# Optimization experiments

Measured on AMD Instinct MI355X. Metric: run time of the kernel, lower is better.

Reference implementation:

```python
import jax, jax.numpy as jnp
import numpy as np

INF = 100000000.0
STRIDES = [8, 16, 32, 64, 128]
REGRESS_RANGES = [(-1.0, 64.0), (64.0, 128.0), (128.0, 256.0), (256.0, 512.0), (512.0, INF)]
IMG = 1024
RADIUS = 1.5
BACKGROUND = 80
NUM_GTS = 512


def setup_inputs() -> dict:
    key = jax.random.key(0)
    k1, k2, k3 = jax.random.split(key, 3)
    # valid gt boxes: centers in image, sizes 10..300, xyxy clipped to image
    cxcy = jax.random.uniform(k1, (NUM_GTS, 2), minval=0.0, maxval=float(IMG))
    wh = jax.random.uniform(k2, (NUM_GTS, 2), minval=10.0, maxval=300.0)
    x1y1 = jnp.clip(cxcy - wh / 2, 0.0, float(IMG))
    x2y2 = jnp.clip(cxcy + wh / 2, 0.0, float(IMG))
    gt_bboxes = jnp.concatenate([x1y1, x2y2], axis=-1)
    gt_labels = jax.random.randint(k3, (NUM_GTS,), 0, BACKGROUND)
    pts, rr, st = [], [], []
    for s, (lo, hi) in zip(STRIDES, REGRESS_RANGES):
        h = w = IMG // s
        y, x = np.meshgrid(np.arange(h), np.arange(w), indexing='ij')
        p = np.stack([x.reshape(-1) * s, y.reshape(-1) * s], axis=-1) + s // 2
        pts.append(p.astype(np.float32))
        rr.append(np.tile(np.array([lo, hi], np.float32), (h * w, 1)))
        st.append(np.full((h * w,), s * RADIUS, np.float32))
    points = jnp.asarray(np.concatenate(pts, 0))          # [N, 2]
    regress_ranges = jnp.asarray(np.concatenate(rr, 0))   # [N, 2]
    strides_pts = jnp.asarray(np.concatenate(st, 0))      # [N]
    return {"points": points, "regress_ranges": regress_ranges,
            "strides_pts": strides_pts, "gt_bboxes": gt_bboxes, "gt_labels": gt_labels}


def reference(points, regress_ranges, strides_pts, gt_bboxes, gt_labels):
    # FCOSTarget._get_target_single (center_sampling=True, no ignore boxes)
    N = points.shape[0]
    xs = points[:, 0:1]  # [N,1]
    ys = points[:, 1:2]
    areas = (gt_bboxes[:, 2] - gt_bboxes[:, 0]) * (gt_bboxes[:, 3] - gt_bboxes[:, 1])  # [G]
    # point-to-box distances, [N,G,4] = (left, top, right, bottom)
    l = xs - gt_bboxes[None, :, 0]
    t = ys - gt_bboxes[None, :, 1]
    r = gt_bboxes[None, :, 2] - xs
    b = gt_bboxes[None, :, 3] - ys
    bbox_targets = jnp.stack([l, t, r, b], axis=-1)  # [N,G,4]
    # center sampling: shrink gt box to stride*radius window around its center
    cx = (gt_bboxes[None, :, 0] + gt_bboxes[None, :, 2]) * 0.5  # [1,G]
    cy = (gt_bboxes[None, :, 1] + gt_bboxes[None, :, 3]) * 0.5
    rad = strides_pts[:, None]  # [N,1], already stride * radius
    x0 = jnp.maximum(cx - rad, gt_bboxes[None, :, 0])
    y0 = jnp.maximum(cy - rad, gt_bboxes[None, :, 1])
    x1 = jnp.minimum(cx + rad, gt_bboxes[None, :, 2])
    y1 = jnp.minimum(cy + rad, gt_bboxes[None, :, 3])
    center_bbox = jnp.stack([xs - x0, ys - y0, x1 - xs, y1 - ys], axis=-1)  # [N,G,4]
    inside_gt_bbox_mask = center_bbox.min(axis=-1) > 0  # [N,G]
    max_regress_distance = bbox_targets.max(axis=-1)  # [N,G]
    inside_regress_range = ((max_regress_distance >= regress_ranges[:, 0:1]) &
                            (max_regress_distance <= regress_ranges[:, 1:2]))
    # masked argmin over gt areas
    areas_masked = jnp.where(inside_gt_bbox_mask & inside_regress_range, areas[None, :], INF)
    min_area = areas_masked.min(axis=1)        # [N]
    min_area_inds = areas_masked.argmin(axis=1)  # [N]
    labels = jnp.where(min_area == INF, BACKGROUND, gt_labels[min_area_inds])
    bt = jnp.take_along_axis(bbox_targets, min_area_inds[:, None, None], axis=1)[:, 0, :]  # [N,4]
    label_weights = jnp.ones((N,), jnp.float32)
    return labels, bt, label_weights
```

## Files before the change

### kernel.cpp

```cpp
#include <hip/hip_runtime.h>

#define INF_AREA 100000000.0f
#define BACKGROUND_LBL 80
#define MAX_GTS 512
#define SPLIT 8

__global__ __launch_bounds__(256) void fcos_target_kernel(
    const float* __restrict__ points,
    const float* __restrict__ regress_ranges,
    const float* __restrict__ strides_pts,
    const float* __restrict__ gt_bboxes,
    const int*   __restrict__ gt_labels,
    float* __restrict__ out,
    int N, int M)
{
    __shared__ float4 sbox[MAX_GTS];
    __shared__ float4 saux[MAX_GTS];

    const float4* gtb4 = reinterpret_cast<const float4*>(gt_bboxes);
    for (int j = threadIdx.x; j < M; j += blockDim.x) {
        float4 b = gtb4[j];
        sbox[j] = b;
        float4 aux;
        aux.x = (b.z - b.x) * (b.w - b.y);
        aux.y = (b.x + b.z) * 0.5f;
        aux.z = (b.y + b.w) * 0.5f;
        aux.w = __int_as_float(gt_labels[j]);
        saux[j] = aux;
    }
    __syncthreads();

    int tid = blockIdx.x * blockDim.x + threadIdx.x;
    int i   = tid >> 3;
    int sub = tid & (SPLIT - 1);
    if (i >= N) return;

    float x   = points[i * 2 + 0];
    float y   = points[i * 2 + 1];
    float rr0 = regress_ranges[i * 2 + 0];
    float rr1 = regress_ranges[i * 2 + 1];
    float rad = strides_pts[i];

    float minA   = INF_AREA;
    int   minIdx = sub;

    for (int j = sub; j < M; j += SPLIT) {
        float4 bx = sbox[j];
        float4 ax = saux[j];
        float l = x - bx.x, t = y - bx.y, r = bx.z - x, b = bx.w - y;
        float mr = fmaxf(fmaxf(l, t), fmaxf(r, b));
        bool in_range = (mr >= rr0) && (mr <= rr1);
        float x0 = fmaxf(ax.y - rad, bx.x);
        float y0 = fmaxf(ax.z - rad, bx.y);
        float x1 = fminf(ax.y + rad, bx.z);
        float y1 = fminf(ax.z + rad, bx.w);
        float cmin = fminf(fminf(x - x0, y - y0), fminf(x1 - x, y1 - y));
        float a = (in_range && (cmin > 0.0f)) ? ax.x : INF_AREA;
        if (a < minA) { minA = a; minIdx = j; }
    }

    for (int off = 1; off < SPLIT; off <<= 1) {
        float oA = __shfl_xor(minA, off);
        int   oI = __shfl_xor(minIdx, off);
        if (oA < minA || (oA == minA && oI < minIdx)) { minA = oA; minIdx = oI; }
    }

    if (sub == 0) {
        float4 bb = sbox[minIdx];
        int lab = (minA == INF_AREA) ? BACKGROUND_LBL : __float_as_int(saux[minIdx].w);
        out[i] = (float)lab;
        float* bt = out + N + (size_t)i * 4;
        bt[0] = x - bb.x;
        bt[1] = y - bb.y;
        bt[2] = bb.z - x;
        bt[3] = bb.w - y;
        out[5 * N + i] = 1.0f;
    }
}

extern "C" void kernel_launch(void* const* d_in, const int* in_sizes, int n_in,
                              void* d_out, int out_size, void* d_ws, size_t ws_size,
                              hipStream_t stream) {
    const float* points         = (const float*)d_in[0];
    const float* regress_ranges = (const float*)d_in[1];
    const float* strides_pts    = (const float*)d_in[2];
    const float* gt_bboxes      = (const float*)d_in[3];
    const int*   gt_labels      = (const int*)d_in[4];
    float* out = (float*)d_out;

    int N = in_sizes[0] / 2;
    int M = in_sizes[3] / 4;

    int block = 256;
    long long total = (long long)N * SPLIT;
    int grid = (int)((total + block - 1) / block);
    fcos_target_kernel<<<grid, block, 0, stream>>>(
        points, regress_ranges, strides_pts, gt_bboxes, gt_labels, out, N, M);
}
```

Baseline: 73.58 us.

## Split GT scan across 32 lanes, recompute aux inline, vectorize target store

Each point's search over GT boxes is now split across 32 lanes instead of 8, so each block covers fewer points and the shuffle reduction gets deeper. The shared auxiliary array (area, center, label) is dropped: area and center are recomputed per iteration from the box, and the label is read from global memory. The loop is unrolled by 4 and the bbox target is written as one float4 store. This cuts shared-memory traffic and per-thread serial work at the cost of extra ALU per iteration and more redundant per-point loads, since 32 lanes now load the same point data.

```diff
diff --git a/kernel.cpp b/kernel.cpp
--- a/kernel.cpp
+++ b/kernel.cpp
@@ -3,7 +3,7 @@
 #define INF_AREA 100000000.0f
 #define BACKGROUND_LBL 80
 #define MAX_GTS 512
-#define SPLIT 8
+#define SPLIT 32
 
 __global__ __launch_bounds__(256) void fcos_target_kernel(
     const float* __restrict__ points,
@@ -15,23 +15,14 @@
     int N, int M)
 {
     __shared__ float4 sbox[MAX_GTS];
-    __shared__ float4 saux[MAX_GTS];
 
     const float4* gtb4 = reinterpret_cast<const float4*>(gt_bboxes);
-    for (int j = threadIdx.x; j < M; j += blockDim.x) {
-        float4 b = gtb4[j];
-        sbox[j] = b;
-        float4 aux;
-        aux.x = (b.z - b.x) * (b.w - b.y);
-        aux.y = (b.x + b.z) * 0.5f;
-        aux.z = (b.y + b.w) * 0.5f;
-        aux.w = __int_as_float(gt_labels[j]);
-        saux[j] = aux;
-    }
+    for (int j = threadIdx.x; j < M; j += blockDim.x)
+        sbox[j] = gtb4[j];
     __syncthreads();
 
     int tid = blockIdx.x * blockDim.x + threadIdx.x;
-    int i   = tid >> 3;
+    int i   = tid >> 5;
     int sub = tid & (SPLIT - 1);
     if (i >= N) return;
 
@@ -44,18 +35,20 @@
     float minA   = INF_AREA;
     int   minIdx = sub;
 
+    #pragma unroll 4
     for (int j = sub; j < M; j += SPLIT) {
         float4 bx = sbox[j];
-        float4 ax = saux[j];
         float l = x - bx.x, t = y - bx.y, r = bx.z - x, b = bx.w - y;
         float mr = fmaxf(fmaxf(l, t), fmaxf(r, b));
         bool in_range = (mr >= rr0) && (mr <= rr1);
-        float x0 = fmaxf(ax.y - rad, bx.x);
-        float y0 = fmaxf(ax.z - rad, bx.y);
-        float x1 = fminf(ax.y + rad, bx.z);
-        float y1 = fminf(ax.z + rad, bx.w);
+        float cx = (bx.x + bx.z) * 0.5f;
+        float cy = (bx.y + bx.w) * 0.5f;
+        float x0 = fmaxf(cx - rad, bx.x);
+        float y0 = fmaxf(cy - rad, bx.y);
+        float x1 = fminf(cx + rad, bx.z);
+        float y1 = fminf(cy + rad, bx.w);
         float cmin = fminf(fminf(x - x0, y - y0), fminf(x1 - x, y1 - y));
-        float a = (in_range && (cmin > 0.0f)) ? ax.x : INF_AREA;
+        float a = (in_range && (cmin > 0.0f)) ? (bx.z - bx.x) * (bx.w - bx.y) : INF_AREA;
         if (a < minA) { minA = a; minIdx = j; }
     }
 
@@ -67,14 +60,11 @@
 
     if (sub == 0) {
         float4 bb = sbox[minIdx];
-        int lab = (minA == INF_AREA) ? BACKGROUND_LBL : __float_as_int(saux[minIdx].w);
+        int lab = (minA == INF_AREA) ? BACKGROUND_LBL : gt_labels[minIdx];
         out[i] = (float)lab;
-        float* bt = out + N + (size_t)i * 4;
-        bt[0] = x - bb.x;
-        bt[1] = y - bb.y;
-        bt[2] = bb.z - x;
-        bt[3] = bb.w - y;
-        out[5 * N + i] = 1.0f;
+        float4 bt = make_float4(x - bb.x, y - bb.y, bb.z - x, bb.w - y);
+        *reinterpret_cast<float4*>(out + N + (size_t)i * 4) = bt;
+        out[5 * (size_t)N + i] = 1.0f;
     }
 }
 
```

Measured after the change: 72.25 us. About the same (-1.8%).
